# Kernel optimization log

Hardware: AMD Instinct MI355X
Metric: run time of the kernel (lower is better)

The kernel has to match this reference:

```python
import jax, jax.numpy as jnp
import numpy as np

# Dimensions (see shape_source): B=4, fine grid 8x8 windows of 16x16 tokens,
# pooled by 4x4 -> global grid 32x32 -> 2x2 windows of 16x16 tokens.
B, H, W, M, C, NH = 4, 8, 8, 16, 256, 8
HD = C // NH
GW = 2  # global window grid (2x2)


def _ln(x, g, b):
    m = x.mean(-1, keepdims=True)
    v = ((x - m) ** 2).mean(-1, keepdims=True)
    return (x - m) / jnp.sqrt(v + 1e-5) * g + b


def _posemb(x, w1, b1, w2):
    # RelativePositionEmbed: MLP(2 -> 512 -> C) over normalized 2D coords.
    N = x.shape[1]
    ctx = int(round(N ** 0.5))
    half = ctx // 2
    r = jnp.arange(ctx, dtype=x.dtype)
    grid = jnp.stack(jnp.meshgrid(r, r, indexing='ij'))  # [2, ctx, ctx]
    coords = ((grid - half) / half).reshape(2, -1).T     # [N, 2]
    return x + jax.nn.relu(coords @ w1 + b1) @ w2


def _mlp(x, w1, b1, w2, b2):
    return jax.nn.gelu(x @ w1 + b1, approximate=False) @ w2 + b2


def _sattn_block(x, ln1g, ln1b, wqkv, bqkv, wo, bo, ln2g, ln2b, mw1, mb1, mw2, mb2):
    # Pre-norm windowed MHSA + MLP (all2all self-attention inside each window).
    bn, N, _ = x.shape
    h = _ln(x, ln1g, ln1b)
    q, k, v = jnp.split(h @ wqkv + bqkv, 3, axis=-1)
    q = q.reshape(bn, N, NH, HD)
    k = k.reshape(bn, N, NH, HD)
    v = v.reshape(bn, N, NH, HD)
    att = jax.nn.softmax(jnp.einsum('bnhd,bmhd->bhnm', q, k) / (HD ** 0.5), axis=-1)
    o = jnp.einsum('bhnm,bmhd->bnhd', att, v).reshape(bn, N, C)
    x = x + o @ wo + bo
    return x + _mlp(_ln(x, ln2g, ln2b), mw1, mb1, mw2, mb2)


def _forward(scale0, scale1, pe_w1, pe_b1, pe_w2, ln1_g, ln1_b, wqkv, bqkv,
             wo, bo, ln2_g, ln2_b, mlp_w1, mlp_b1, mlp_w2, mlp_b2):
    # 1) per-scale relative position embeddings (weight_share=False path)
    x0 = _posemb(scale0, pe_w1[0], pe_b1[0], pe_w2[0])  # [B*64, 256, C]
    x1 = _posemb(scale1, pe_w1[1], pe_b1[1], pe_w2[1])  # [B*4, 256, C]

    # 2) propagate_bottom_up: max-pool each 16x16 window by 4 -> 4x4,
    p = x0.reshape(B * H * W, 4, 4, 4, 4, C).max(axis=(2, 4))  # (r1,p1,r2,p2)->max over p
    p = p.reshape(B, H, W, 4, 4, C).transpose(0, 1, 3, 2, 4, 5).reshape(B, H * 4, W * 4, C)
    l2g = p.reshape(B, GW, M, GW, M, C).transpose(0, 1, 3, 2, 4, 5).reshape(B * GW * GW, M * M, C)
    x1 = x1 + l2g

    # 3) all2all self-attention per scale (coarse to fine order; independent)
    o1 = _sattn_block(x1, ln1_g[1], ln1_b[1], wqkv[1], bqkv[1], wo[1], bo[1],
                      ln2_g[1], ln2_b[1], mlp_w1[1], mlp_b1[1], mlp_w2[1], mlp_b2[1])
    o0 = _sattn_block(x0, ln1_g[0], ln1_b[0], wqkv[0], bqkv[0], wo[0], bo[0],
                      ln2_g[0], ln2_b[0], mlp_w1[0], mlp_b1[0], mlp_w2[0], mlp_b2[0])

    # 4) one2one cross-attention aggregation: each global token queries the
    #    4x4 fine-token region it was pooled from (one-to-one mapping).
    fine = o0.reshape(B, H, W, 4, 4, 4, 4, C).transpose(0, 1, 2, 3, 5, 4, 6, 7)
    fine = fine.reshape(B * H * W * 16, 16, C)  # [B*1024, 16, C], order (b,h,w,r1,r2)
    g = o1.reshape(B, GW, GW, M, M, C).transpose(0, 1, 3, 2, 4, 5).reshape(B, 32, 32, C)
    g = g.reshape(B, H, 4, W, 4, C).transpose(0, 1, 3, 2, 4, 5).reshape(B * H * W * 16, 1, C)

    qn = _ln(g, ln1_g[1], ln1_b[1])
    kn = _ln(fine, ln1_g[1], ln1_b[1])
    wq, wk, wv = jnp.split(wqkv[1], 3, axis=-1)
    bq, bk, bv = jnp.split(bqkv[1], 3)
    q = (qn @ wq + bq).reshape(-1, 1, NH, HD)
    k = (kn @ wk + bk).reshape(-1, 16, NH, HD)
    v = (kn @ wv + bv).reshape(-1, 16, NH, HD)
    att = jax.nn.softmax(jnp.einsum('bnhd,bmhd->bhnm', q, k) / (HD ** 0.5), axis=-1)
    o = jnp.einsum('bhnm,bmhd->bnhd', att, v).reshape(-1, 1, C)
    g = g + o @ wo[1] + bo[1]
    g = g + _mlp(_ln(g, ln2_g[1], ln2_b[1]), mlp_w1[1], mlp_b1[1], mlp_w2[1], mlp_b2[1])

    # back to global window layout [B*4, 256, C]
    g = g.reshape(B, H, W, 4, 4, C).transpose(0, 1, 3, 2, 4, 5).reshape(B, 32, 32, C)
    o1 = g.reshape(B, GW, M, GW, M, C).transpose(0, 1, 3, 2, 4, 5).reshape(B * GW * GW, M * M, C)

    # concat on window axis so the harness sees a single output array
    return jnp.concatenate([o0, o1], axis=0)  # [272, 256, C]


def setup_inputs() -> dict:
    key = jax.random.key(0)
    ks = jax.random.split(key, 8)

    def w(k, shape):
        return jax.random.normal(k, shape, jnp.float32) * 0.02

    return {
        'scale0': jax.random.normal(ks[0], (B * H * W, M * M, C), jnp.float32),
        'scale1': jax.random.normal(ks[1], (B * GW * GW, M * M, C), jnp.float32),
        'pe_w1': w(ks[2], (2, 2, 512)), 'pe_b1': jnp.zeros((2, 512), jnp.float32),
        'pe_w2': w(ks[3], (2, 512, C)),
        'ln1_g': jnp.ones((2, C), jnp.float32), 'ln1_b': jnp.zeros((2, C), jnp.float32),
        'wqkv': w(ks[4], (2, C, 3 * C)), 'bqkv': jnp.zeros((2, 3 * C), jnp.float32),
        'wo': w(ks[5], (2, C, C)), 'bo': jnp.zeros((2, C), jnp.float32),
        'ln2_g': jnp.ones((2, C), jnp.float32), 'ln2_b': jnp.zeros((2, C), jnp.float32),
        'mlp_w1': w(ks[6], (2, C, 4 * C)), 'mlp_b1': jnp.zeros((2, 4 * C), jnp.float32),
        'mlp_w2': w(ks[7], (2, 4 * C, C)), 'mlp_b2': jnp.zeros((2, C), jnp.float32),
    }


def reference(scale0, scale1, pe_w1, pe_b1, pe_w2, ln1_g, ln1_b, wqkv, bqkv,
              wo, bo, ln2_g, ln2_b, mlp_w1, mlp_b1, mlp_w2, mlp_b2):
    return _forward(scale0, scale1, pe_w1, pe_b1, pe_w2, ln1_g, ln1_b, wqkv,
                    bqkv, wo, bo, ln2_g, ln2_b, mlp_w1, mlp_b1, mlp_w2, mlp_b2)
```

## Files before the change

kernel.cpp:

```cpp
#include <hip/hip_runtime.h>
#include <hip/hip_bf16.h>
#include <hip/hip_fp16.h>

#define ROWS0 65536
#define ROWS1 4096

typedef _Float16 half8 __attribute__((ext_vector_type(8)));
typedef _Float16 half4_t __attribute__((ext_vector_type(4)));
typedef float floatx4 __attribute__((ext_vector_type(4)));

#define LDSP(p) ((__attribute__((address_space(3))) void*)(p))
#define GLBP(p) ((const __attribute__((address_space(1))) void*)(p))

__device__ __forceinline__ float gelu_f(float x) {
    return 0.5f * x * (1.0f + erff(x * 0.70710678118654752f));
}

__global__ __launch_bounds__(256) void pe_kernel(
    const float* __restrict__ w1, const float* __restrict__ b1,
    const float* __restrict__ w2, float* __restrict__ pe)
{
    __shared__ float hid[512];
    int blk = blockIdx.x;
    int s = blk >> 8, n = blk & 255;
    int i = n >> 4, j = n & 15;
    float c0 = (i - 8) * 0.125f;
    float c1 = (j - 8) * 0.125f;
    int t = threadIdx.x;
    for (int hh = t; hh < 512; hh += 256) {
        float hv = c0 * w1[s * 1024 + hh] + c1 * w1[s * 1024 + 512 + hh] + b1[s * 512 + hh];
        hid[hh] = fmaxf(hv, 0.f);
    }
    __syncthreads();
    float o = 0.f;
    const float* w2p = w2 + (size_t)s * 512 * 256 + t;
    #pragma unroll 8
    for (int hh = 0; hh < 512; hh++) o += hid[hh] * w2p[hh * 256];
    pe[(size_t)s * 65536 + n * 256 + t] = o;
}

__global__ __launch_bounds__(256) void add_pe0_kernel(
    const float* __restrict__ s0, const float* __restrict__ pe, float* __restrict__ out)
{
    int row = blockIdx.x, c = threadIdx.x;
    out[(size_t)row * 256 + c] = s0[(size_t)row * 256 + c] + pe[(row & 255) * 256 + c];
}

__global__ __launch_bounds__(256) void pool_kernel(
    const float* __restrict__ x0, const float* __restrict__ s1,
    const float* __restrict__ pe1, float* __restrict__ x1out)
{
    int w1 = blockIdx.x >> 8, n1 = blockIdx.x & 255, c = threadIdx.x;
    int b = w1 >> 2, wy = (w1 >> 1) & 1, wx = w1 & 1;
    int ty = n1 >> 4, tx = n1 & 15;
    int gy = wy * 16 + ty, gx = wx * 16 + tx;
    int h = gy >> 2, r1 = gy & 3, w = gx >> 2, r2 = gx & 3;
    int fw = (b * 8 + h) * 8 + w;
    const float* base = x0 + ((size_t)fw * 256 + r1 * 64 + r2 * 4) * 256 + c;
    float mv = -1e30f;
    #pragma unroll
    for (int p1 = 0; p1 < 4; p1++)
        #pragma unroll
        for (int p2 = 0; p2 < 4; p2++)
            mv = fmaxf(mv, base[(p1 * 16 + p2) * 256]);
    size_t oidx = ((size_t)w1 * 256 + n1) * 256 + c;
    x1out[oidx] = s1[oidx] + pe1[n1 * 256 + c] + mv;
}

__global__ __launch_bounds__(256) void ln16_kernel(
    const float* __restrict__ X, const float* __restrict__ g,
    const float* __restrict__ b, _Float16* __restrict__ Y)
{
    __shared__ float smr[4];
    int row = blockIdx.x, t = threadIdx.x;
    float x = X[(size_t)row * 256 + t];
    float v = x;
    for (int o = 32; o; o >>= 1) v += __shfl_down(v, o);
    if ((t & 63) == 0) smr[t >> 6] = v;
    __syncthreads();
    float mean = (smr[0] + smr[1] + smr[2] + smr[3]) * (1.0f / 256.0f);
    __syncthreads();
    float d = x - mean;
    float vv = d * d;
    for (int o = 32; o; o >>= 1) vv += __shfl_down(vv, o);
    if ((t & 63) == 0) smr[t >> 6] = vv;
    __syncthreads();
    float var = (smr[0] + smr[1] + smr[2] + smr[3]) * (1.0f / 256.0f);
    float inv = 1.0f / sqrtf(var + 1e-5f);
    Y[(size_t)row * 256 + t] = (_Float16)(d * inv * g[t] + b[t]);
}

__global__ __launch_bounds__(256) void transposeW_kernel(
    const float* __restrict__ src, _Float16* __restrict__ dst, int K, int N)
{
    __shared__ float t[32][33];
    int k0 = blockIdx.y * 32, n0 = blockIdx.x * 32;
    int tx = threadIdx.x & 31, ty = threadIdx.x >> 5;
    for (int r = ty; r < 32; r += 8) t[r][tx] = src[(size_t)(k0 + r) * N + n0 + tx];
    __syncthreads();
    for (int r = ty; r < 32; r += 8) dst[(size_t)(n0 + r) * K + k0 + tx] = (_Float16)t[tx][r];
}

template<int ACT, int RES, int OUT16>
__global__ __launch_bounds__(256) void hgemm_kernel(
    const _Float16* __restrict__ A, const _Float16* __restrict__ Bw,
    const float* __restrict__ bias, const float* __restrict__ Res,
    void* __restrict__ Yv, int M, int N, int K)
{
    __shared__ alignas(16) _Float16 smem[2 * 128 * 64];
    _Float16* As = smem;
    _Float16* Bs = smem + 8192;
    int tid = threadIdx.x;

    int gx = N >> 7;
    int nwg = gx * (M >> 7);
    int q8 = nwg >> 3;
    int wg = (blockIdx.x & 7) * q8 + (blockIdx.x >> 3);
    int m0 = (wg / gx) << 7, n0 = (wg % gx) << 7;

    int wave = tid >> 6, lane = tid & 63;
    int wr = wave >> 1, wc = wave & 1;
    floatx4 acc[4][4] = {};

    for (int k0 = 0; k0 < K; k0 += 64) {
        #pragma unroll
        for (int p = 0; p < 4; p++) {
            int s = tid + (p << 8);
            int row = s >> 3, phys = s & 7;
            int logc = phys ^ (row & 7);
            const _Float16* ga = A + (size_t)(m0 + row) * K + k0 + logc * 8;
            __builtin_amdgcn_global_load_lds(GLBP(ga), LDSP(&As[s * 8]), 16, 0, 0);
            const _Float16* gb = Bw + (size_t)(n0 + row) * K + k0 + logc * 8;
            __builtin_amdgcn_global_load_lds(GLBP(gb), LDSP(&Bs[s * 8]), 16, 0, 0);
        }
        __syncthreads();
        int r = lane & 15, c = lane >> 4;
        #pragma unroll
        for (int ks = 0; ks < 2; ks++) {
            half8 af[4], bf[4];
            #pragma unroll
            for (int i = 0; i < 4; i++) {
                int ra = wr * 64 + i * 16 + r;
                af[i] = *(const half8*)&As[ra * 64 + (((ks << 2) | c) ^ (ra & 7)) * 8];
                int rb = wc * 64 + i * 16 + r;
                bf[i] = *(const half8*)&Bs[rb * 64 + (((ks << 2) | c) ^ (rb & 7)) * 8];
            }
            #pragma unroll
            for (int i = 0; i < 4; i++)
                #pragma unroll
                for (int j = 0; j < 4; j++)
                    acc[i][j] = __builtin_amdgcn_mfma_f32_16x16x32_f16(af[i], bf[j], acc[i][j], 0, 0, 0);
        }
        __syncthreads();
    }

    int r = lane & 15, qrow = lane >> 4;
    if (OUT16) {
        _Float16* sth = smem + wave * 1024;
        #pragma unroll
        for (int i = 0; i < 4; i++) {
            #pragma unroll
            for (int j = 0; j < 4; j++) {
                float bj = bias[n0 + wc * 64 + j * 16 + r];
                #pragma unroll
                for (int reg = 0; reg < 4; reg++) {
                    float v = acc[i][j][reg] + bj;
                    if (ACT) v = gelu_f(v);
                    sth[(qrow * 4 + reg) * 64 + j * 16 + r] = (_Float16)v;
                }
            }
            #pragma unroll
            for (int p = 0; p < 2; p++) {
                int row = p * 8 + (lane >> 3);
                half8 hv = *(const half8*)&sth[row * 64 + (lane & 7) * 8];
                *(half8*)((_Float16*)Yv + (size_t)(m0 + wr * 64 + i * 16 + row) * N
                          + n0 + wc * 64 + (lane & 7) * 8) = hv;
            }
        }
    } else {
        float* stf = (float*)smem + wave * 1024;
        #pragma unroll
        for (int i = 0; i < 4; i++) {
            #pragma unroll
            for (int j = 0; j < 4; j++) {
                float bj = bias[n0 + wc * 64 + j * 16 + r];
                #pragma unroll
                for (int reg = 0; reg < 4; reg++) {
                    float v = acc[i][j][reg] + bj;
                    if (ACT) v = gelu_f(v);
                    stf[(qrow * 4 + reg) * 64 + j * 16 + r] = v;
                }
            }
            #pragma unroll
            for (int p = 0; p < 4; p++) {
                int row = p * 4 + (lane >> 4);
                float4 fv = *(const float4*)&stf[row * 64 + (lane & 15) * 4];
                size_t ga = (size_t)(m0 + wr * 64 + i * 16 + row) * N
                            + n0 + wc * 64 + (lane & 15) * 4;
                if (RES) {
                    float4 rv = *(const float4*)(Res + ga);
                    fv.x += rv.x; fv.y += rv.y; fv.z += rv.z; fv.w += rv.w;
                }
                *(float4*)((float*)Yv + ga) = fv;
            }
        }
    }
}

__global__ __launch_bounds__(256) void attn_mfma_kernel(
    const _Float16* __restrict__ qkv, _Float16* __restrict__ out)
{
    __shared__ alignas(16) _Float16 Klds[8192];
    __shared__ alignas(16) _Float16 Qlds[8192];
    __shared__ alignas(16) _Float16 VT[8192];
    __shared__ alignas(16) _Float16 Pl[4][4096];

    int tid = threadIdx.x;
    int win = blockIdx.x, head = blockIdx.y;
    int w = tid >> 6, lane = tid & 63;
    int r = lane & 15, h = lane >> 4;

    {
        const _Float16* base = qkv + ((size_t)(win * 256 + tid)) * 768 + head * 32;
        half8 qv[4], kv[4], vv[4];
        #pragma unroll
        for (int c = 0; c < 4; c++) {
            qv[c] = *(const half8*)(base + c * 8);
            kv[c] = *(const half8*)(base + 256 + c * 8);
            vv[c] = *(const half8*)(base + 512 + c * 8);
        }
        int rowbase = (tid >> 1) * 64;
        #pragma unroll
        for (int c = 0; c < 4; c++) {
            int phys = (((tid & 1) << 2) + c) ^ ((tid >> 1) & 7);
            *(half8*)&Qlds[rowbase + phys * 8] = qv[c];
            *(half8*)&Klds[rowbase + phys * 8] = kv[c];
        }
        #pragma unroll
        for (int d = 0; d < 32; d++)
            VT[d * 256 + (((tid >> 3) ^ (d & 7)) << 3) + (tid & 7)] = vv[d >> 3][d & 7];
    }
    __syncthreads();

    half8 vf[2][8];
    #pragma unroll
    for (int dc = 0; dc < 2; dc++)
        #pragma unroll
        for (int kc2 = 0; kc2 < 8; kc2++)
            vf[dc][kc2] = *(const half8*)&VT[(dc * 16 + r) * 256 + ((((kc2 << 2) + h) ^ (r & 7)) << 3)];

    const floatx4 zf = {0.f, 0.f, 0.f, 0.f};
    int physa = (((r & 1) << 2) + h) ^ ((r >> 1) & 7);

    for (int g = 0; g < 4; g++) {
        int qg = (w << 2) + g;
        half8 qb = *(const half8*)&Qlds[((qg << 3) + (r >> 1)) * 64 + physa * 8];
        floatx4 s[16];
        #pragma unroll
        for (int kc = 0; kc < 16; kc++) {
            half8 ka = *(const half8*)&Klds[((kc << 3) + (r >> 1)) * 64 + physa * 8];
            s[kc] = __builtin_amdgcn_mfma_f32_16x16x32_f16(ka, qb, zf, 0, 0, 0);
        }
        float m = -1e30f;
        #pragma unroll
        for (int kc = 0; kc < 16; kc++)
            #pragma unroll
            for (int e = 0; e < 4; e++) m = fmaxf(m, s[kc][e]);
        m = fmaxf(m, __shfl_xor(m, 16));
        m = fmaxf(m, __shfl_xor(m, 32));
        float l = 0.f;
        #pragma unroll
        for (int kc = 0; kc < 16; kc++)
            #pragma unroll
            for (int e = 0; e < 4; e++) {
                float p = __expf((s[kc][e] - m) * 0.17677669529663687f);
                s[kc][e] = p;
                l += p;
            }
        l += __shfl_xor(l, 16);
        l += __shfl_xor(l, 32);
        float inv = 1.0f / l;
        #pragma unroll
        for (int kc = 0; kc < 16; kc++) {
            half4_t pk;
            pk[0] = (_Float16)s[kc][0]; pk[1] = (_Float16)s[kc][1];
            pk[2] = (_Float16)s[kc][2]; pk[3] = (_Float16)s[kc][3];
            *(half4_t*)&Pl[w][r * 256 + ((((kc << 1) + (h >> 1)) ^ (r & 7)) << 3) + ((h & 1) << 2)] = pk;
        }
        floatx4 o0 = zf, o1 = zf;
        #pragma unroll
        for (int kc2 = 0; kc2 < 8; kc2++) {
            half8 pb = *(const half8*)&Pl[w][r * 256 + ((((kc2 << 2) + h) ^ (r & 7)) << 3)];
            o0 = __builtin_amdgcn_mfma_f32_16x16x32_f16(vf[0][kc2], pb, o0, 0, 0, 0);
            o1 = __builtin_amdgcn_mfma_f32_16x16x32_f16(vf[1][kc2], pb, o1, 0, 0, 0);
        }
        #pragma unroll
        for (int dc = 0; dc < 2; dc++) {
            floatx4 o = dc ? o1 : o0;
            half4_t oh;
            #pragma unroll
            for (int e = 0; e < 4; e++) oh[e] = (_Float16)(o[e] * inv);
            *(half4_t*)&Pl[w][(r >> 1) * 64 + (((((r & 1) << 2) + (dc << 1) + (h >> 1)) ^ ((r >> 1) & 7)) << 3) + ((h & 1) << 2)] = oh;
        }
        int q2 = lane >> 2, c2 = lane & 3;
        half8 ov = *(const half8*)&Pl[w][(q2 >> 1) * 64 + (((((q2 & 1) << 2) + c2) ^ ((q2 >> 1) & 7)) << 3)];
        *(half8*)(out + ((size_t)(win * 256 + qg * 16 + q2)) * 256 + head * 32 + c2 * 8) = ov;
    }
}

__global__ __launch_bounds__(128) void cross_attn_kernel(
    const _Float16* __restrict__ Qb, const _Float16* __restrict__ KV,
    _Float16* __restrict__ Ob, int fw0)
{
    __shared__ float att_s[8][16];
    int t = threadIdx.x;
    int lw = blockIdx.x >> 4;
    int sub = blockIdx.x & 15;
    int r1 = sub >> 2, r2 = sub & 3;
    int gi = (fw0 + lw) * 16 + sub;
    int h = t >> 4, m = t & 15;
    int p1 = m >> 2, p2 = m & 3;
    int lr = lw * 256 + r1 * 64 + p1 * 16 + r2 * 4 + p2;
    const half8* qp = (const half8*)(Qb + (size_t)gi * 256 + h * 32);
    const half8* kp = (const half8*)(KV + (size_t)lr * 512 + h * 32);
    float sc = 0.f;
    #pragma unroll
    for (int d8 = 0; d8 < 4; d8++) {
        half8 qv = qp[d8], kv = kp[d8];
        #pragma unroll
        for (int j = 0; j < 8; j++) sc += (float)qv[j] * (float)kv[j];
    }
    sc *= 0.17677669529663687f;
    float mx = sc;
    for (int o = 8; o; o >>= 1) mx = fmaxf(mx, __shfl_xor(mx, o));
    float e = __expf(sc - mx);
    float ssum = e;
    for (int o = 8; o; o >>= 1) ssum += __shfl_xor(ssum, o);
    att_s[h][m] = e / ssum;
    __syncthreads();
    int dg = t & 15;
    int d0 = dg * 2;
    float o0 = 0.f, o1 = 0.f;
    #pragma unroll
    for (int mm = 0; mm < 16; mm++) {
        int pp1 = mm >> 2, pp2 = mm & 3;
        int lrr = lw * 256 + r1 * 64 + pp1 * 16 + r2 * 4 + pp2;
        const _Float16* vp = KV + (size_t)lrr * 512 + 256 + h * 32;
        float a = att_s[h][mm];
        o0 += a * (float)vp[d0];
        o1 += a * (float)vp[d0 + 1];
    }
    Ob[(size_t)gi * 256 + h * 32 + d0]     = (_Float16)o0;
    Ob[(size_t)gi * 256 + h * 32 + d0 + 1] = (_Float16)o1;
}

__global__ __launch_bounds__(256) void gather_g_kernel(
    const float* __restrict__ o1, float* __restrict__ G)
{
    int gi = blockIdx.x, c = threadIdx.x;
    int b = gi >> 10, rem = gi & 1023;
    int h = rem >> 7, w = (rem >> 4) & 7, r1 = (rem >> 2) & 3, r2 = rem & 3;
    int gy = h * 4 + r1, gx = w * 4 + r2;
    int w1 = (b * 2 + (gy >> 4)) * 2 + (gx >> 4);
    int n1 = (gy & 15) * 16 + (gx & 15);
    G[(size_t)gi * 256 + c] = o1[((size_t)w1 * 256 + n1) * 256 + c];
}

__global__ __launch_bounds__(256) void scatter_g_kernel(
    const float* __restrict__ G, float* __restrict__ o1)
{
    int gi = blockIdx.x, c = threadIdx.x;
    int b = gi >> 10, rem = gi & 1023;
    int h = rem >> 7, w = (rem >> 4) & 7, r1 = (rem >> 2) & 3, r2 = rem & 3;
    int gy = h * 4 + r1, gx = w * 4 + r2;
    int w1 = (b * 2 + (gy >> 4)) * 2 + (gx >> 4);
    int n1 = (gy & 15) * 16 + (gx & 15);
    o1[((size_t)w1 * 256 + n1) * 256 + c] = G[(size_t)gi * 256 + c];
}

extern "C" void kernel_launch(void* const* d_in, const int* in_sizes, int n_in,
                              void* d_out, int out_size, void* d_ws, size_t ws_size,
                              hipStream_t stream)
{
    const float* scale0 = (const float*)d_in[0];
    const float* scale1 = (const float*)d_in[1];
    const float* pe_w1  = (const float*)d_in[2];
    const float* pe_b1  = (const float*)d_in[3];
    const float* pe_w2  = (const float*)d_in[4];
    const float* ln1_g  = (const float*)d_in[5];
    const float* ln1_b  = (const float*)d_in[6];
    const float* wqkv   = (const float*)d_in[7];
    const float* bqkv   = (const float*)d_in[8];
    const float* wo     = (const float*)d_in[9];
    const float* bo     = (const float*)d_in[10];
    const float* ln2_g  = (const float*)d_in[11];
    const float* ln2_b  = (const float*)d_in[12];
    const float* mw1    = (const float*)d_in[13];
    const float* mb1    = (const float*)d_in[14];
    const float* mw2    = (const float*)d_in[15];
    const float* mb2    = (const float*)d_in[16];
    float* out = (float*)d_out;
    char* arena = (char*)d_ws;

    float*    PE     = (float*)arena;              arena += 131072 * 4;
    float*    G      = (float*)arena;              arena += (size_t)4096 * 256 * 4;
    _Float16* Q16    = (_Float16*)arena;           arena += (size_t)4096 * 256 * 2;
    _Float16* OX16   = (_Float16*)arena;           arena += (size_t)4096 * 256 * 2;
    _Float16* wqkvT  = (_Float16*)arena;           arena += (size_t)2 * 768 * 256 * 2;
    _Float16* woT    = (_Float16*)arena;           arena += (size_t)2 * 256 * 256 * 2;
    _Float16* mw1T   = (_Float16*)arena;           arena += (size_t)2 * 1024 * 256 * 2;
    _Float16* mw2T   = (_Float16*)arena;           arena += (size_t)2 * 256 * 1024 * 2;
    size_t fixed_bytes = (size_t)(arena - (char*)d_ws);

    int R = 8192;
    if (fixed_bytes + (size_t)65536 * 4608 <= ws_size) R = 65536;
    else if (fixed_bytes + (size_t)32768 * 4608 <= ws_size) R = 32768;
    else if (fixed_bytes + (size_t)16384 * 4608 <= ws_size) R = 16384;
    int NC = 65536 / R;
    int CW = R / 256;

    _Float16* bufH16 = (_Float16*)arena;           arena += (size_t)R * 256 * 2;
    _Float16* qkv16  = (_Float16*)arena;           arena += (size_t)R * 768 * 2;
    _Float16* hid16  = (_Float16*)arena;           arena += (size_t)R * 1024 * 2;
    _Float16* o16    = (_Float16*)arena;

    auto hgemm = [&](const _Float16* A, const _Float16* Bw, const float* bias,
                     const float* Res, void* Y, int M, int N, int K, int act) {
        int nwg = (N >> 7) * (M >> 7);
        if (act)           hgemm_kernel<1, 0, 1><<<nwg, 256, 0, stream>>>(A, Bw, bias, nullptr, Y, M, N, K);
        else if (Res)      hgemm_kernel<0, 1, 0><<<nwg, 256, 0, stream>>>(A, Bw, bias, Res, Y, M, N, K);
        else               hgemm_kernel<0, 0, 1><<<nwg, 256, 0, stream>>>(A, Bw, bias, nullptr, Y, M, N, K);
    };

    auto sattn = [&](float* x, int Mrows, int nw, int s) {
        ln16_kernel<<<Mrows, 256, 0, stream>>>(x, ln1_g + s * 256, ln1_b + s * 256, bufH16);
        hgemm(bufH16, wqkvT + (size_t)s * 196608, bqkv + s * 768, nullptr, qkv16, Mrows, 768, 256, 0);
        attn_mfma_kernel<<<dim3(nw, 8), 256, 0, stream>>>(qkv16, o16);
        hgemm(o16, woT + (size_t)s * 65536, bo + s * 256, x, x, Mrows, 256, 256, 0);
        ln16_kernel<<<Mrows, 256, 0, stream>>>(x, ln2_g + s * 256, ln2_b + s * 256, bufH16);
        hgemm(bufH16, mw1T + (size_t)s * 262144, mb1 + s * 1024, nullptr, hid16, Mrows, 1024, 256, 1);
        hgemm(hid16, mw2T + (size_t)s * 262144, mb2 + s * 256, x, x, Mrows, 256, 1024, 0);
    };

    float* o1sec = out + (size_t)ROWS0 * 256;

    transposeW_kernel<<<dim3(768 / 32, 256 / 32), 256, 0, stream>>>(wqkv, wqkvT, 256, 768);
    transposeW_kernel<<<dim3(768 / 32, 256 / 32), 256, 0, stream>>>(wqkv + 196608, wqkvT + 196608, 256, 768);
    transposeW_kernel<<<dim3(256 / 32, 256 / 32), 256, 0, stream>>>(wo, woT, 256, 256);
    transposeW_kernel<<<dim3(256 / 32, 256 / 32), 256, 0, stream>>>(wo + 65536, woT + 65536, 256, 256);
    transposeW_kernel<<<dim3(1024 / 32, 256 / 32), 256, 0, stream>>>(mw1, mw1T, 256, 1024);
    transposeW_kernel<<<dim3(1024 / 32, 256 / 32), 256, 0, stream>>>(mw1 + 262144, mw1T + 262144, 256, 1024);
    transposeW_kernel<<<dim3(256 / 32, 1024 / 32), 256, 0, stream>>>(mw2, mw2T, 1024, 256);
    transposeW_kernel<<<dim3(256 / 32, 1024 / 32), 256, 0, stream>>>(mw2 + 262144, mw2T + 262144, 1024, 256);

    pe_kernel<<<512, 256, 0, stream>>>(pe_w1, pe_b1, pe_w2, PE);
    add_pe0_kernel<<<ROWS0, 256, 0, stream>>>(scale0, PE, out);
    pool_kernel<<<ROWS1, 256, 0, stream>>>(out, scale1, PE + 65536, o1sec);

    sattn(o1sec, ROWS1, 16, 1);
    for (int c = 0; c < NC; c++)
        sattn(out + (size_t)c * R * 256, R, CW, 0);

    gather_g_kernel<<<4096, 256, 0, stream>>>(o1sec, G);
    ln16_kernel<<<4096, 256, 0, stream>>>(G, ln1_g + 256, ln1_b + 256, bufH16);
    hgemm(bufH16, wqkvT + 196608, bqkv + 768, nullptr, Q16, 4096, 256, 256, 0);
    for (int c = 0; c < NC; c++) {
        float* xch = out + (size_t)c * R * 256;
        ln16_kernel<<<R, 256, 0, stream>>>(xch, ln1_g + 256, ln1_b + 256, bufH16);
        hgemm(bufH16, wqkvT + 196608 + 65536, bqkv + 768 + 256, nullptr, qkv16, R, 512, 256, 0);
        cross_attn_kernel<<<CW * 16, 128, 0, stream>>>(Q16, qkv16, OX16, c * CW);
    }
    hgemm(OX16, woT + 65536, bo + 256, G, G, 4096, 256, 256, 0);
    ln16_kernel<<<4096, 256, 0, stream>>>(G, ln2_g + 256, ln2_b + 256, bufH16);
    hgemm(bufH16, mw1T + 262144, mb1 + 1024, nullptr, hid16, 4096, 1024, 256, 1);
    hgemm(hid16, mw2T + 262144, mb2 + 256, G, G, 4096, 256, 1024, 0);
    scatter_g_kernel<<<4096, 256, 0, stream>>>(G, o1sec);
}
```

Baseline: 914.6 us.

## Double-buffer GEMM k-tiles, pad epilogue staging, use tanh-form GELU approximation

The GEMM main loop now uses a K-step of 32 with two LDS buffers, so the global->LDS load of the next tile is issued before the MFMAs on the current tile. The goal is to overlap memory latency with compute, at the cost of more loop iterations for the same K. The epilogue staging rows are padded (72 halves / 68 floats) to reduce LDS bank conflicts. Exact erf GELU is replaced with a sigmoid-based tanh approximation, which is cheaper but changes numerics relative to the exact-GELU reference.

```diff
diff --git a/kernel.cpp b/kernel.cpp
--- a/kernel.cpp
+++ b/kernel.cpp
@@ -13,7 +13,8 @@
 #define GLBP(p) ((const __attribute__((address_space(1))) void*)(p))
 
 __device__ __forceinline__ float gelu_f(float x) {
-    return 0.5f * x * (1.0f + erff(x * 0.70710678118654752f));
+    float t = x * (1.595769122f + 0.071354816f * x * x);
+    return x / (1.0f + __expf(-t));
 }
 
 __global__ __launch_bounds__(256) void pe_kernel(
@@ -107,9 +108,7 @@
     const float* __restrict__ bias, const float* __restrict__ Res,
     void* __restrict__ Yv, int M, int N, int K)
 {
-    __shared__ alignas(16) _Float16 smem[2 * 128 * 64];
-    _Float16* As = smem;
-    _Float16* Bs = smem + 8192;
+    __shared__ alignas(16) _Float16 smem[4 * 4096];
     int tid = threadIdx.x;
 
     int gx = N >> 7;
@@ -120,43 +119,52 @@
 
     int wave = tid >> 6, lane = tid & 63;
     int wr = wave >> 1, wc = wave & 1;
+    int r = lane & 15, c = lane >> 4;
     floatx4 acc[4][4] = {};
 
-    for (int k0 = 0; k0 < K; k0 += 64) {
-        #pragma unroll
-        for (int p = 0; p < 4; p++) {
+    const int NT = K >> 5;
+
+    auto stage = [&](int buf, int t) {
+        int k0 = t << 5;
+        #pragma unroll
+        for (int p = 0; p < 2; p++) {
             int s = tid + (p << 8);
-            int row = s >> 3, phys = s & 7;
-            int logc = phys ^ (row & 7);
+            int row = s >> 2, phys = s & 3;
+            int logc = phys ^ (row & 3);
             const _Float16* ga = A + (size_t)(m0 + row) * K + k0 + logc * 8;
-            __builtin_amdgcn_global_load_lds(GLBP(ga), LDSP(&As[s * 8]), 16, 0, 0);
+            __builtin_amdgcn_global_load_lds(GLBP(ga), LDSP(&smem[buf * 4096 + s * 8]), 16, 0, 0);
             const _Float16* gb = Bw + (size_t)(n0 + row) * K + k0 + logc * 8;
-            __builtin_amdgcn_global_load_lds(GLBP(gb), LDSP(&Bs[s * 8]), 16, 0, 0);
-        }
+            __builtin_amdgcn_global_load_lds(GLBP(gb), LDSP(&smem[8192 + buf * 4096 + s * 8]), 16, 0, 0);
+        }
+    };
+
+    stage(0, 0);
+    __syncthreads();
+    int cur = 0;
+    for (int t = 0; t < NT; t++) {
+        if (t + 1 < NT) stage(cur ^ 1, t + 1);
+        const _Float16* As = &smem[cur * 4096];
+        const _Float16* Bs = &smem[8192 + cur * 4096];
+        half8 af[4], bf[4];
+        #pragma unroll
+        for (int i = 0; i < 4; i++) {
+            int ra = wr * 64 + i * 16 + r;
+            af[i] = *(const half8*)&As[ra * 32 + ((c ^ (ra & 3)) << 3)];
+            int rb = wc * 64 + i * 16 + r;
+            bf[i] = *(const half8*)&Bs[rb * 32 + ((c ^ (rb & 3)) << 3)];
+        }
+        #pragma unroll
+        for (int i = 0; i < 4; i++)
+            #pragma unroll
+            for (int j = 0; j < 4; j++)
+                acc[i][j] = __builtin_amdgcn_mfma_f32_16x16x32_f16(af[i], bf[j], acc[i][j], 0, 0, 0);
         __syncthreads();
-        int r = lane & 15, c = lane >> 4;
-        #pragma unroll
-        for (int ks = 0; ks < 2; ks++) {
-            half8 af[4], bf[4];
-            #pragma unroll
-            for (int i = 0; i < 4; i++) {
-                int ra = wr * 64 + i * 16 + r;
-                af[i] = *(const half8*)&As[ra * 64 + (((ks << 2) | c) ^ (ra & 7)) * 8];
-                int rb = wc * 64 + i * 16 + r;
-                bf[i] = *(const half8*)&Bs[rb * 64 + (((ks << 2) | c) ^ (rb & 7)) * 8];
-            }
-            #pragma unroll
-            for (int i = 0; i < 4; i++)
-                #pragma unroll
-                for (int j = 0; j < 4; j++)
-                    acc[i][j] = __builtin_amdgcn_mfma_f32_16x16x32_f16(af[i], bf[j], acc[i][j], 0, 0, 0);
-        }
-        __syncthreads();
-    }
-
-    int r = lane & 15, qrow = lane >> 4;
+        cur ^= 1;
+    }
+
+    int qrow = lane >> 4;
     if (OUT16) {
-        _Float16* sth = smem + wave * 1024;
+        _Float16* sth = smem + wave * 1152;
         #pragma unroll
         for (int i = 0; i < 4; i++) {
             #pragma unroll
@@ -166,19 +174,19 @@
                 for (int reg = 0; reg < 4; reg++) {
                     float v = acc[i][j][reg] + bj;
                     if (ACT) v = gelu_f(v);
-                    sth[(qrow * 4 + reg) * 64 + j * 16 + r] = (_Float16)v;
+                    sth[(qrow * 4 + reg) * 72 + j * 16 + r] = (_Float16)v;
                 }
             }
             #pragma unroll
             for (int p = 0; p < 2; p++) {
                 int row = p * 8 + (lane >> 3);
-                half8 hv = *(const half8*)&sth[row * 64 + (lane & 7) * 8];
+                half8 hv = *(const half8*)&sth[row * 72 + (lane & 7) * 8];
                 *(half8*)((_Float16*)Yv + (size_t)(m0 + wr * 64 + i * 16 + row) * N
                           + n0 + wc * 64 + (lane & 7) * 8) = hv;
             }
         }
     } else {
-        float* stf = (float*)smem + wave * 1024;
+        float* stf = (float*)smem + wave * 1088;
         #pragma unroll
         for (int i = 0; i < 4; i++) {
             #pragma unroll
@@ -188,13 +196,13 @@
                 for (int reg = 0; reg < 4; reg++) {
                     float v = acc[i][j][reg] + bj;
                     if (ACT) v = gelu_f(v);
-                    stf[(qrow * 4 + reg) * 64 + j * 16 + r] = v;
+                    stf[(qrow * 4 + reg) * 68 + j * 16 + r] = v;
                 }
             }
             #pragma unroll
             for (int p = 0; p < 4; p++) {
                 int row = p * 4 + (lane >> 4);
-                float4 fv = *(const float4*)&stf[row * 64 + (lane & 15) * 4];
+                float4 fv = *(const float4*)&stf[row * 68 + (lane & 15) * 4];
                 size_t ga = (size_t)(m0 + wr * 64 + i * 16 + row) * N
                             + n0 + wc * 64 + (lane & 15) * 4;
                 if (RES) {
```

Measured after the change: 865.1 us. 5.4% less time.
